# Kernel tuning notes

Hardware: AMD Instinct MI355X
Metric: run time of the kernel (lower is better)

## Reference

```python
import jax, jax.numpy as jnp
import numpy as np

N_BINS = 15


def setup_inputs() -> dict:
    key = jax.random.key(0)
    k1, k2 = jax.random.split(key)
    N, C = 2_000_000, 128
    u = jax.random.uniform(k1, (N, C), dtype=jnp.float32)
    probs = u / jnp.sum(u, axis=1, keepdims=True)  # valid softmax-like scores
    labels = jax.random.randint(k2, (N,), 0, C, dtype=jnp.int32)
    return {"probs": probs, "labels": labels}


def reference(probs, labels):
    # confidences, predictions = torch.max(probs, 1)
    conf = jnp.max(probs, axis=1)            # [N]
    preds = jnp.argmax(probs, axis=1)        # [N]
    acc = (preds == labels).astype(probs.dtype)

    # bin membership: bin_lower < conf <= bin_upper, boundaries = linspace(0,1,n_bins+1)
    boundaries = jnp.linspace(0.0, 1.0, N_BINS + 1).astype(probs.dtype)
    # searchsorted 'left' gives i with boundaries[i-1] < conf <= boundaries[i]
    bin_idx = jnp.searchsorted(boundaries, conf, side="left") - 1  # [N], -1 if conf==0
    valid = (bin_idx >= 0) & (bin_idx < N_BINS)
    seg = jnp.where(valid, bin_idx, N_BINS)  # invalid samples -> overflow bin
    w = valid.astype(probs.dtype)

    counts = jax.ops.segment_sum(w, seg, num_segments=N_BINS + 1)[:N_BINS]
    conf_sum = jax.ops.segment_sum(conf * w, seg, num_segments=N_BINS + 1)[:N_BINS]
    acc_sum = jax.ops.segment_sum(acc * w, seg, num_segments=N_BINS + 1)[:N_BINS]

    n_total = probs.shape[0]
    prop_in_bin = counts / n_total
    nonempty = counts > 0
    denom = jnp.maximum(counts, 1.0)
    avg_conf = conf_sum / denom
    avg_acc = acc_sum / denom
    gaps = jnp.where(nonempty, jnp.abs(avg_conf - avg_acc) * prop_in_bin, 0.0)
    ece = jnp.sum(gaps)
    return ece.reshape(1)
```

## Files before the change

kernel.cpp:

```cpp
#include <hip/hip_runtime.h>
#include <math.h>

#define N_BINS 15

constexpr int BLOCK = 256;
constexpr int NWAVES = BLOCK / 64;
constexpr int GRID_MAX = 2048;
constexpr int S2_THREADS = 768;

__global__ __launch_bounds__(BLOCK, 8) void ece_partial_kernel(
    const float* __restrict__ probs,
    const int*   __restrict__ labels,
    float*       __restrict__ partial,
    int N, int grid)
{
    const int tid   = threadIdx.x;
    const int lane  = tid & 63;
    const int wv    = tid >> 6;
    const int sub   = lane & 7;
    const int grp   = lane >> 3;
    const int myBin = lane & 15;

    const long long gw        = (long long)blockIdx.x * NWAVES + wv;
    const long long W         = (long long)grid * NWAVES;
    const long long rowStride = W * 8;
    const int e0 = sub * 4;

    float cnt = 0.f, cs = 0.f, as_ = 0.f;

    for (long long row0 = gw * 8; row0 < (long long)N; row0 += rowStride) {
        const long long row = row0 + grp;
        const bool rv = row < (long long)N;

        float4 a = make_float4(0.f,0.f,0.f,0.f), b = a, c = a, d = a;
        int lbl = -1;
        if (rv) {
            const float* rp = probs + ((size_t)row << 7) + e0;
            a = *reinterpret_cast<const float4*>(rp);
            b = *reinterpret_cast<const float4*>(rp + 32);
            c = *reinterpret_cast<const float4*>(rp + 64);
            d = *reinterpret_cast<const float4*>(rp + 96);
            lbl = labels[row];
        }

        float m = a.x; int idx = e0;
#define UPD(val, id) { float _v = (val); int _i = (id); if (_v > m) { m = _v; idx = _i; } }
        UPD(a.y, e0+1)  UPD(a.z, e0+2)  UPD(a.w, e0+3)
        UPD(b.x, e0+32) UPD(b.y, e0+33) UPD(b.z, e0+34) UPD(b.w, e0+35)
        UPD(c.x, e0+64) UPD(c.y, e0+65) UPD(c.z, e0+66) UPD(c.w, e0+67)
        UPD(d.x, e0+96) UPD(d.y, e0+97) UPD(d.z, e0+98) UPD(d.w, e0+99)
#undef UPD

#pragma unroll
        for (int off = 4; off >= 1; off >>= 1) {
            float om = __shfl_xor(m, off);
            int   oi = __shfl_xor(idx, off);
            if (om > m || (om == m && oi < idx)) { m = om; idx = oi; }
        }
        const float conf = m;
        const int   accv = (idx == lbl) ? 1 : 0;

        const float gf = conf * 15.0f;
        const int j0 = (int)gf;
        int bin;
        if      ((float)(j0 + 1) * (1.0f / 15.0f) < conf) bin = j0 + 1;
        else if ((float)j0       * (1.0f / 15.0f) < conf) bin = j0;
        else                                              bin = j0 - 1;

        const int   pk    = ((bin + 1) & 31) | (accv << 8);
        const float conf1 = __shfl_xor(conf, 8);
        const int   pk1   = __shfl_xor(pk, 8);
        const int   bin1  = (pk1 & 31) - 1;
        const int   acc1  = pk1 >> 8;

        const float s0 = (bin  == myBin) ? 1.f : 0.f;
        const float s1 = (bin1 == myBin) ? 1.f : 0.f;
        cnt += s0 + s1;
        cs  += s0 * conf + s1 * conf1;
        as_ += s0 * (float)accv + s1 * (float)acc1;
    }

    cnt += __shfl_xor(cnt, 16); cs += __shfl_xor(cs, 16); as_ += __shfl_xor(as_, 16);
    cnt += __shfl_xor(cnt, 32); cs += __shfl_xor(cs, 32); as_ += __shfl_xor(as_, 32);

    __shared__ float sh[NWAVES][16][3];
    if (lane < 16) {
        sh[wv][lane][0] = cnt;
        sh[wv][lane][1] = cs;
        sh[wv][lane][2] = as_;
    }
    __syncthreads();

    if (tid < 48) {
        const int bin = tid / 3, comp = tid % 3;
        float s = 0.f;
#pragma unroll
        for (int w2 = 0; w2 < NWAVES; ++w2) s += sh[w2][bin][comp];
        partial[(size_t)tid * grid + blockIdx.x] = s;
    }
}

__global__ __launch_bounds__(S2_THREADS) void ece_final_kernel(
    const float* __restrict__ partial, float* __restrict__ out,
    int grid, int N)
{
    __shared__ double s2[48][16];
    __shared__ double sb[48];
    const int t = threadIdx.x;
    const int comp = t >> 4, sub = t & 15;

    double s = 0.0;
    for (int b = sub; b < grid; b += 16)
        s += (double)partial[(size_t)comp * grid + b];
    s2[comp][sub] = s;
    __syncthreads();

    if (t < 48) {
        double v = 0.0;
#pragma unroll
        for (int k = 0; k < 16; ++k) v += s2[t][k];
        sb[t] = v;
    }
    __syncthreads();

    if (t == 0) {
        double ece = 0.0;
        for (int bin = 0; bin < N_BINS; ++bin) {
            const double c0 = sb[bin * 3 + 0];
            const double c1 = sb[bin * 3 + 1];
            const double c2 = sb[bin * 3 + 2];
            if (c0 > 0.0)
                ece += fabs(c1 / c0 - c2 / c0) * (c0 / (double)N);
        }
        out[0] = (float)ece;
    }
}

extern "C" void kernel_launch(void* const* d_in, const int* in_sizes, int n_in,
                              void* d_out, int out_size, void* d_ws, size_t ws_size,
                              hipStream_t stream)
{
    const float* probs  = (const float*)d_in[0];
    const int*   labels = (const int*)d_in[1];
    const int N = in_sizes[1];
    float* out = (float*)d_out;
    float* partial = (float*)d_ws;

    int grid = GRID_MAX;
    const size_t need_per_block = 48 * sizeof(float);
    if ((size_t)grid * need_per_block > ws_size) {
        grid = (int)(ws_size / need_per_block);
        if (grid < 1) grid = 1;
    }

    ece_partial_kernel<<<grid, BLOCK, 0, stream>>>(probs, labels, partial, N, grid);
    ece_final_kernel<<<1, S2_THREADS, 0, stream>>>(partial, out, grid, N);
}
```

Measured before the change: 221.5 us.

## Prefetch next row tile in registers and replace argmax with a label-probability compare

The row loop becomes software-pipelined: each iteration issues the float4 loads for the next strided row group before reducing the current one, aiming to keep more memory requests in flight. The argmax index tracking and its tie-breaking shuffle are dropped. Accuracy is now decided by loading probs[row][label] and checking whether it equals the row max. This changes behaviour on exact ties, where it counts a hit that the first-index argmax would not. Grid size and the launch-bounds occupancy hint are lowered to make room for the extra registers the prefetch buffers need.

```diff
diff --git a/kernel.cpp b/kernel.cpp
--- a/kernel.cpp
+++ b/kernel.cpp
@@ -5,10 +5,10 @@
 
 constexpr int BLOCK = 256;
 constexpr int NWAVES = BLOCK / 64;
-constexpr int GRID_MAX = 2048;
+constexpr int GRID_MAX = 1536;
 constexpr int S2_THREADS = 768;
 
-__global__ __launch_bounds__(BLOCK, 8) void ece_partial_kernel(
+__global__ __launch_bounds__(BLOCK, 6) void ece_partial_kernel(
     const float* __restrict__ probs,
     const int*   __restrict__ labels,
     float*       __restrict__ partial,
@@ -20,20 +20,20 @@
     const int sub   = lane & 7;
     const int grp   = lane >> 3;
     const int myBin = lane & 15;
+    const int e0    = sub * 4;
 
     const long long gw        = (long long)blockIdx.x * NWAVES + wv;
-    const long long W         = (long long)grid * NWAVES;
-    const long long rowStride = W * 8;
-    const int e0 = sub * 4;
+    const long long rowStride = (long long)grid * NWAVES * 8;
 
     float cnt = 0.f, cs = 0.f, as_ = 0.f;
 
-    for (long long row0 = gw * 8; row0 < (long long)N; row0 += rowStride) {
+    long long row0 = gw * 8;
+    float4 a = make_float4(0,0,0,0), b = a, c = a, d = a;
+    int lbl = 0; bool rv = false;
+
+    if (row0 < (long long)N) {
         const long long row = row0 + grp;
-        const bool rv = row < (long long)N;
-
-        float4 a = make_float4(0.f,0.f,0.f,0.f), b = a, c = a, d = a;
-        int lbl = -1;
+        rv = row < (long long)N;
         if (rv) {
             const float* rp = probs + ((size_t)row << 7) + e0;
             a = *reinterpret_cast<const float4*>(rp);
@@ -42,42 +42,59 @@
             d = *reinterpret_cast<const float4*>(rp + 96);
             lbl = labels[row];
         }
+    }
 
-        float m = a.x; int idx = e0;
-#define UPD(val, id) { float _v = (val); int _i = (id); if (_v > m) { m = _v; idx = _i; } }
-        UPD(a.y, e0+1)  UPD(a.z, e0+2)  UPD(a.w, e0+3)
-        UPD(b.x, e0+32) UPD(b.y, e0+33) UPD(b.z, e0+34) UPD(b.w, e0+35)
-        UPD(c.x, e0+64) UPD(c.y, e0+65) UPD(c.z, e0+66) UPD(c.w, e0+67)
-        UPD(d.x, e0+96) UPD(d.y, e0+97) UPD(d.z, e0+98) UPD(d.w, e0+99)
-#undef UPD
+    while (row0 < (long long)N) {
+        const long long row = row0 + grp;
 
-#pragma unroll
-        for (int off = 4; off >= 1; off >>= 1) {
-            float om = __shfl_xor(m, off);
-            int   oi = __shfl_xor(idx, off);
-            if (om > m || (om == m && oi < idx)) { m = om; idx = oi; }
+        const float pl = rv ? probs[((size_t)row << 7) + (size_t)lbl] : -1.0f;
+
+        const long long nrow0 = row0 + rowStride;
+        float4 a2 = make_float4(0,0,0,0), b2 = a2, c2 = a2, d2 = a2;
+        int lbl2 = 0; bool rv2 = false;
+        if (nrow0 < (long long)N) {
+            const long long nr = nrow0 + grp;
+            rv2 = nr < (long long)N;
+            if (rv2) {
+                const float* rp = probs + ((size_t)nr << 7) + e0;
+                a2 = *reinterpret_cast<const float4*>(rp);
+                b2 = *reinterpret_cast<const float4*>(rp + 32);
+                c2 = *reinterpret_cast<const float4*>(rp + 64);
+                d2 = *reinterpret_cast<const float4*>(rp + 96);
+                lbl2 = labels[nr];
+            }
         }
+
+        float m = fmaxf(
+            fmaxf(fmaxf(fmaxf(a.x, a.y), fmaxf(a.z, a.w)),
+                  fmaxf(fmaxf(b.x, b.y), fmaxf(b.z, b.w))),
+            fmaxf(fmaxf(fmaxf(c.x, c.y), fmaxf(c.z, c.w)),
+                  fmaxf(fmaxf(d.x, d.y), fmaxf(d.z, d.w))));
+
+        #pragma unroll
+        for (int off = 4; off >= 1; off >>= 1)
+            m = fmaxf(m, __shfl_xor(m, off));
         const float conf = m;
-        const int   accv = (idx == lbl) ? 1 : 0;
 
-        const float gf = conf * 15.0f;
-        const int j0 = (int)gf;
+        const int j0 = (int)(conf * 15.0f);
         int bin;
         if      ((float)(j0 + 1) * (1.0f / 15.0f) < conf) bin = j0 + 1;
         else if ((float)j0       * (1.0f / 15.0f) < conf) bin = j0;
         else                                              bin = j0 - 1;
 
-        const int   pk    = ((bin + 1) & 31) | (accv << 8);
+        const int acc = (pl == conf) ? 1 : 0;
+
         const float conf1 = __shfl_xor(conf, 8);
-        const int   pk1   = __shfl_xor(pk, 8);
-        const int   bin1  = (pk1 & 31) - 1;
-        const int   acc1  = pk1 >> 8;
+        const int   pk1   = __shfl_xor((bin & 31) | (acc << 8), 8);
 
-        const float s0 = (bin  == myBin) ? 1.f : 0.f;
-        const float s1 = (bin1 == myBin) ? 1.f : 0.f;
-        cnt += s0 + s1;
-        cs  += s0 * conf + s1 * conf1;
-        as_ += s0 * (float)accv + s1 * (float)acc1;
+        const bool s0 = (bin == myBin);
+        const bool s1 = ((pk1 & 31) == myBin);
+        cnt += (s0 ? 1.f : 0.f) + (s1 ? 1.f : 0.f);
+        cs  += (s0 ? conf : 0.f) + (s1 ? conf1 : 0.f);
+        as_ += ((s0 && acc) ? 1.f : 0.f) + ((s1 && (pk1 >> 8)) ? 1.f : 0.f);
+
+        row0 = nrow0;
+        a = a2; b = b2; c = c2; d = d2; lbl = lbl2; rv = rv2;
     }
 
     cnt += __shfl_xor(cnt, 16); cs += __shfl_xor(cs, 16); as_ += __shfl_xor(as_, 16);
@@ -92,10 +109,10 @@
     __syncthreads();
 
     if (tid < 48) {
-        const int bin = tid / 3, comp = tid % 3;
+        const int bin2 = tid / 3, comp = tid % 3;
         float s = 0.f;
-#pragma unroll
-        for (int w2 = 0; w2 < NWAVES; ++w2) s += sh[w2][bin][comp];
+        #pragma unroll
+        for (int w2 = 0; w2 < NWAVES; ++w2) s += sh[w2][bin2][comp];
         partial[(size_t)tid * grid + blockIdx.x] = s;
     }
 }
@@ -110,14 +127,14 @@
     const int comp = t >> 4, sub = t & 15;
 
     double s = 0.0;
-    for (int b = sub; b < grid; b += 16)
-        s += (double)partial[(size_t)comp * grid + b];
+    for (int bk = sub; bk < grid; bk += 16)
+        s += (double)partial[(size_t)comp * grid + bk];
     s2[comp][sub] = s;
     __syncthreads();
 
     if (t < 48) {
         double v = 0.0;
-#pragma unroll
+        #pragma unroll
         for (int k = 0; k < 16; ++k) v += s2[t][k];
         sb[t] = v;
     }
```

Result: faster. 201.0 us (-9.2%).
